# Performance work log

Hardware: AMD Instinct MI355X
Metric: run time of the kernel (lower is better)

The kernel has to match this reference:

```python
import jax, jax.numpy as jnp
import numpy as np

B, D, NSTEPS = 256, 4096, 30
DT = 0.5  # args.dt

def rho(x):
    # hard-sigmoid activation used throughout the EP repo
    return jnp.clip(x, 0.0, 1.0)

def setup_inputs() -> dict:
    key = jax.random.key(0)
    k_s3, k_w0, k_w2, k_w4 = jax.random.split(key, 4)
    sc = 1.0 / np.sqrt(D)
    W0 = jax.random.normal(k_w0, (D, D), jnp.float32) * sc  # w[0]: layer1 -> layer0
    W2 = jax.random.normal(k_w2, (D, D), jnp.float32) * sc  # w[2]: layer2 -> layer1
    W4 = jax.random.normal(k_w4, (D, D), jnp.float32) * sc  # w[4]: data  -> layer2
    return {
        "s0": jnp.zeros((B, D), jnp.float32),
        "s1": jnp.zeros((B, D), jnp.float32),
        "s2": jnp.zeros((B, D), jnp.float32),
        "s3": jax.random.uniform(k_s3, (B, D), jnp.float32),  # clamped data layer in [0,1]
        "W0": W0, "b0": jnp.zeros((D,), jnp.float32),
        "W1": W0.T,  # w[2i+1].weight = w[2i].weight.T at init (tied transpose)
        "W2": W2, "b2": jnp.zeros((D,), jnp.float32),
        "W3": W2.T,
        "W4": W4, "b4": jnp.zeros((D,), jnp.float32),
        "N": NSTEPS,
    }

def reference(s0, s1, s2, s3, W0, b0, W1, W2, b2, W3, W4, b4, N):
    # non-spiking EP free-phase relaxation (beta=0), no_clamp=False
    top_in = rho(s3) @ W4.T + b4  # s3 is clamped data; constant across steps

    def step(carry, _):
        c0, c1, c2 = carry
        r0, r1, r2 = rho(c0), rho(c1), rho(c2)
        ds0 = -c0 + r1 @ W0.T + b0
        ds1 = -c1 + r2 @ W2.T + b2 + r0 @ W1.T
        ds2 = -c2 + top_in + r1 @ W3.T
        n0 = jnp.clip(c0 + DT * ds0, 0.0, 1.0)
        n1 = jnp.clip(c1 + DT * ds1, 0.0, 1.0)
        n2 = jnp.clip(c2 + DT * ds2, 0.0, 1.0)
        return (n0, n1, n2), None

    (s0, s1, s2), _ = jax.lax.scan(step, (s0, s1, s2), None, length=N)
    return jnp.stack([s0, s1, s2])  # [3, B, D]
```

## Files before the change

### kernel.cpp

```cpp
#include <hip/hip_runtime.h>


typedef unsigned short u16;
typedef __attribute__((ext_vector_type(8))) _Float16 f16x8;
typedef __attribute__((ext_vector_type(4))) float f32x4;

constexpr int Bb = 256, Dd = 4096, NSTEPS = 30;
constexpr long BD = (long)Bb * Dd;
constexpr long DD = (long)Dd * Dd;
constexpr int BM = 32;
constexpr int NBUF = 3;
constexpr int BUFB = 20480;

__device__ inline u16 f2h(float f) { union { _Float16 h; u16 u; } v; v.h = (_Float16)f; return v.u; }
__device__ inline float h2f(u16 b) { union { u16 u; _Float16 h; } v; v.u = b; return (float)v.h; }

__device__ inline void gl_lds16(const u16* g, void* l) {
    __builtin_amdgcn_global_load_lds(
        (const __attribute__((address_space(1))) void*)g,
        (__attribute__((address_space(3))) void*)l, 16, 0, 0);
}

__global__ __launch_bounds__(256)
void convert_w(const float* __restrict__ src, u16* __restrict__ dst, long n) {
    long i = (long)blockIdx.x * blockDim.x + threadIdx.x;
    const long stride = (long)gridDim.x * blockDim.x;
    for (long v = i; v < (n >> 2); v += stride) {
        float4 x = ((const float4*)src)[v];
        ushort4 o; o.x = f2h(x.x); o.y = f2h(x.y); o.z = f2h(x.z); o.w = f2h(x.w);
        ((ushort4*)dst)[v] = o;
    }
}

__global__ __launch_bounds__(256)
void convert_s(const float* __restrict__ src, u16* __restrict__ hi, u16* __restrict__ lo, long n) {
    long i = (long)blockIdx.x * blockDim.x + threadIdx.x;
    const long stride = (long)gridDim.x * blockDim.x;
    for (long v = i; v < (n >> 2); v += stride) {
        float4 x = ((const float4*)src)[v];
        float a[4] = {x.x, x.y, x.z, x.w};
        ushort4 oh, ol;
        u16* ph = (u16*)&oh; u16* pl = (u16*)&ol;
        #pragma unroll
        for (int j = 0; j < 4; ++j) {
            float c = fminf(fmaxf(a[j], 0.f), 1.f);
            u16 hb = f2h(c);
            ph[j] = hb;
            pl[j] = f2h(c - h2f(hb));
        }
        ((ushort4*)hi)[v] = oh;
        ((ushort4*)lo)[v] = ol;
    }
}

__device__ inline void stage_tile(const u16* aH, const u16* aL, const u16* W,
                                  int m0, int n0, int k, char* buf, int wv, int lane)
{
    const int srow = lane >> 2;
    const int koff = (((lane & 3) ^ ((lane >> 3) & 3)) << 3);
    const u16* aBase = (wv < 2) ? aH : aL;
    const int aRow = ((wv & 1) << 4) + srow;
    char* aDst = buf + ((wv >> 1) << 11) + ((wv & 1) << 10);
    gl_lds16(aBase + (size_t)(m0 + aRow) * Dd + k + koff, aDst);
    const u16* wSrc = W + (size_t)(n0 + 64 * wv + srow) * Dd + k + koff;
    char* wDst = buf + 4096 + wv * 4096;
    #pragma unroll
    for (int c = 0; c < 4; ++c)
        gl_lds16(wSrc + (size_t)(16 * c) * Dd, wDst + (c << 10));
}

template<bool FULL>
__device__ inline void run_gemm(const u16* aH, const u16* aL, const u16* W,
                                const int m0, const int n0, char* smem,
                                const float* bias, const float* add,
                                const float* pF, const u16* pH, const u16* pL,
                                float* outF, u16* oH, u16* oL, const long zOff)
{
    const int lane = threadIdx.x & 63, wv = threadIdx.x >> 6;
    f32x4 acc[2][4] = {};
    constexpr int nk = 128;

    stage_tile(aH, aL, W, m0, n0, 0,  smem,        wv, lane);
    stage_tile(aH, aL, W, m0, n0, 32, smem + BUFB, wv, lane);

    int ib = 0;
    const int r16 = lane & 15;
    const int qoff = (((lane >> 4) ^ ((r16 >> 1) & 3)) << 4);

    for (int kk = 0; kk < nk; ++kk) {
        if (kk + 1 < nk) asm volatile("s_waitcnt vmcnt(5)" ::: "memory");
        else             asm volatile("s_waitcnt vmcnt(0)" ::: "memory");
        __builtin_amdgcn_s_barrier();
        asm volatile("" ::: "memory");

        if (kk + 2 < nk) {
            int ib2 = ib + 2; if (ib2 >= NBUF) ib2 -= NBUF;
            stage_tile(aH, aL, W, m0, n0, (kk + 2) << 5, smem + ib2 * BUFB, wv, lane);
        }

        const char* buf = smem + ib * BUFB;
        ++ib; if (ib == NBUF) ib = 0;

        f16x8 ah[2], al[2], wf[4];
        #pragma unroll
        for (int i = 0; i < 2; ++i) {
            ah[i] = *(const f16x8*)(buf + ((16 * i + r16) << 6) + qoff);
            al[i] = *(const f16x8*)(buf + 2048 + ((16 * i + r16) << 6) + qoff);
        }
        #pragma unroll
        for (int j = 0; j < 4; ++j)
            wf[j] = *(const f16x8*)(buf + 4096 + ((64 * wv + 16 * j + r16) << 6) + qoff);

        __builtin_amdgcn_s_setprio(1);
        #pragma unroll
        for (int j = 0; j < 4; ++j) {
            #pragma unroll
            for (int i = 0; i < 2; ++i) {
                acc[i][j] = __builtin_amdgcn_mfma_f32_16x16x32_f16(ah[i], wf[j], acc[i][j], 0, 0, 0);
                acc[i][j] = __builtin_amdgcn_mfma_f32_16x16x32_f16(al[i], wf[j], acc[i][j], 0, 0, 0);
            }
        }
        __builtin_amdgcn_s_setprio(0);
    }

    const int q = lane >> 4;
    #pragma unroll
    for (int j = 0; j < 4; ++j) {
        const int n = n0 + 64 * wv + 16 * j + r16;
        #pragma unroll
        for (int i = 0; i < 2; ++i) {
            #pragma unroll
            for (int r = 0; r < 4; ++r) {
                const int m = m0 + 16 * i + q * 4 + r;
                const size_t idx = (size_t)m * Dd + n;
                float e = acc[i][j][r];
                if (!FULL) {
                    outF[idx] = bias ? e + bias[n] : e;
                } else {
                    if (bias) e += bias[n];
                    if (add)  e += add[idx];
                    const float p = pF ? pF[zOff + idx] : (h2f(pH[zOff + idx]) + h2f(pL[zOff + idx]));
                    float v = 0.5f * p + 0.5f * e;
                    v = fminf(fmaxf(v, 0.f), 1.f);
                    const u16 hb = f2h(v);
                    oH[zOff + idx] = hb;
                    oL[zOff + idx] = f2h(v - h2f(hb));
                    if (outF) outF[zOff + idx] = v;
                }
            }
        }
    }
}

template<int MODE>
__global__ __launch_bounds__(256, 2)
void step_mfma(const u16* __restrict__ sH, const u16* __restrict__ sL,
               const u16* __restrict__ W0h, const u16* __restrict__ W1h,
               const u16* __restrict__ W2h, const u16* __restrict__ W3h,
               const float* __restrict__ b0, const float* __restrict__ b2,
               const float* __restrict__ top,
               const float* __restrict__ pF,
               const u16* __restrict__ pH, const u16* __restrict__ pL,
               float* __restrict__ outF,
               u16* __restrict__ oH, u16* __restrict__ oL,
               float* __restrict__ p0, float* __restrict__ p1)
{
    __shared__ __align__(16) char smem[NBUF * BUFB];
    const int id = blockIdx.x;

    if (MODE == 0) {
        const int mt = id >> 4, nt = id & 15;
        run_gemm<false>(sH, sL, W0h, mt * BM, nt * 256, smem, b0, nullptr,
                        nullptr, nullptr, nullptr, outF, nullptr, nullptr, 0);
    } else {
        const int t = id & 127, mt = t >> 4, nt = t & 15;
        const int m0 = mt * BM, n0 = nt * 256;
        if (id < 128) {
            run_gemm<true>(sH + BD, sL + BD, W0h, m0, n0, smem, b0, nullptr,
                           pF, pH, pL, outF, oH, oL, 0);
        } else if (id < 256) {
            run_gemm<false>(sH + 2 * BD, sL + 2 * BD, W2h, m0, n0, smem, b2, nullptr,
                            nullptr, nullptr, nullptr, p0, nullptr, nullptr, 0);
        } else if (id < 384) {
            run_gemm<false>(sH, sL, W1h, m0, n0, smem, nullptr, nullptr,
                            nullptr, nullptr, nullptr, p1, nullptr, nullptr, 0);
        } else {
            run_gemm<true>(sH + BD, sL + BD, W3h, m0, n0, smem, nullptr, top,
                           pF, pH, pL, outF, oH, oL, 2 * BD);
        }
    }
}

__global__ __launch_bounds__(256)
void finish_l1(const float* __restrict__ p0, const float* __restrict__ p1,
               const float* __restrict__ pF,
               const u16* __restrict__ pH, const u16* __restrict__ pL,
               float* __restrict__ outF, u16* __restrict__ oH, u16* __restrict__ oL)
{
    const long v = (long)blockIdx.x * blockDim.x + threadIdx.x;
    float4 a = ((const float4*)p0)[v];
    float4 b = ((const float4*)p1)[v];
    float e[4] = {a.x + b.x, a.y + b.y, a.z + b.z, a.w + b.w};
    float p[4];
    if (pF) {
        float4 pv = ((const float4*)(pF + BD))[v];
        p[0] = pv.x; p[1] = pv.y; p[2] = pv.z; p[3] = pv.w;
    } else {
        ushort4 hv = ((const ushort4*)(pH + BD))[v];
        ushort4 lv = ((const ushort4*)(pL + BD))[v];
        p[0] = h2f(hv.x) + h2f(lv.x); p[1] = h2f(hv.y) + h2f(lv.y);
        p[2] = h2f(hv.z) + h2f(lv.z); p[3] = h2f(hv.w) + h2f(lv.w);
    }
    ushort4 oh, ol; u16* ph = (u16*)&oh; u16* pl = (u16*)&ol;
    float4 ov;
    float* po = (float*)&ov;
    #pragma unroll
    for (int j = 0; j < 4; ++j) {
        float x = 0.5f * p[j] + 0.5f * e[j];
        x = fminf(fmaxf(x, 0.f), 1.f);
        const u16 hb = f2h(x);
        ph[j] = hb;
        pl[j] = f2h(x - h2f(hb));
        po[j] = x;
    }
    ((ushort4*)(oH + BD))[v] = oh;
    ((ushort4*)(oL + BD))[v] = ol;
    if (outF) ((float4*)(outF + BD))[v] = ov;
}

extern "C" void kernel_launch(void* const* d_in, const int* in_sizes, int n_in,
                              void* d_out, int out_size, void* d_ws, size_t ws_size,
                              hipStream_t stream)
{
    const float* s0 = (const float*)d_in[0];
    const float* s1 = (const float*)d_in[1];
    const float* s2 = (const float*)d_in[2];
    const float* s3 = (const float*)d_in[3];
    const float* W0 = (const float*)d_in[4];
    const float* b0 = (const float*)d_in[5];
    const float* W1 = (const float*)d_in[6];
    const float* W2 = (const float*)d_in[7];
    const float* b2 = (const float*)d_in[8];
    const float* W3 = (const float*)d_in[9];
    const float* W4 = (const float*)d_in[10];
    const float* b4 = (const float*)d_in[11];

    float* top = (float*)d_ws;
    u16* u   = (u16*)(top + BD);
    u16* W0h = u;            u16* W1h = u + DD;     u16* W2h = u + 2 * DD;
    u16* W3h = u + 3 * DD;   u16* W4h = u + 4 * DD;
    u16* sHa = u + 5 * DD;
    u16* sLa = sHa + 3 * BD;
    u16* sHb = sLa + 3 * BD;
    u16* sLb = sHb + 3 * BD;
    u16* s3h = sLb + 3 * BD;
    u16* s3l = s3h + BD;
    float* p0 = (float*)W4h;
    float* p1 = p0 + BD;

    float* out = (float*)d_out;
    const dim3 blk(256);
    const dim3 cgrid(512);

    convert_w<<<cgrid, blk, 0, stream>>>(W0, W0h, DD);
    convert_w<<<cgrid, blk, 0, stream>>>(W1, W1h, DD);
    convert_w<<<cgrid, blk, 0, stream>>>(W2, W2h, DD);
    convert_w<<<cgrid, blk, 0, stream>>>(W3, W3h, DD);
    convert_w<<<cgrid, blk, 0, stream>>>(W4, W4h, DD);
    convert_s<<<cgrid, blk, 0, stream>>>(s3, s3h, s3l, BD);
    convert_s<<<cgrid, blk, 0, stream>>>(s0, sHa,          sLa,          BD);
    convert_s<<<cgrid, blk, 0, stream>>>(s1, sHa + BD,     sLa + BD,     BD);
    convert_s<<<cgrid, blk, 0, stream>>>(s2, sHa + 2 * BD, sLa + 2 * BD, BD);

    step_mfma<0><<<dim3(128), blk, 0, stream>>>(
        s3h, s3l, W4h, nullptr, nullptr, nullptr,
        b4, nullptr, nullptr,
        nullptr, nullptr, nullptr,
        top, nullptr, nullptr, nullptr, nullptr);

    for (int t = 0; t < NSTEPS; ++t) {
        const u16* iH = (t & 1) ? sHb : sHa;
        const u16* iL = (t & 1) ? sLb : sLa;
        u16*       vH = (t & 1) ? sHa : sHb;
        u16*       vL = (t & 1) ? sLa : sLb;
        float* oF = (t == NSTEPS - 1) ? out : nullptr;
        const float* pF = nullptr;
        if (t == 0) {
            hipMemcpyAsync(out,          s0, BD * sizeof(float), hipMemcpyDeviceToDevice, stream);
            hipMemcpyAsync(out + BD,     s1, BD * sizeof(float), hipMemcpyDeviceToDevice, stream);
            hipMemcpyAsync(out + 2 * BD, s2, BD * sizeof(float), hipMemcpyDeviceToDevice, stream);
            pF = out;
        }
        step_mfma<1><<<dim3(512), blk, 0, stream>>>(
            iH, iL, W0h, W1h, W2h, W3h, b0, b2, top,
            pF, iH, iL,
            oF, vH, vL, p0, p1);
        finish_l1<<<dim3(BD / 4 / 256), blk, 0, stream>>>(
            p0, p1, pF, iH, iL, oF, vH, vL);
    }
}
```

Baseline: 3.758 ms.

## Load weight fragments directly to registers, stage only activations through LDS

Each wave's private W columns are now loaded straight from global memory into registers, double-buffered across iterations. Only the hi/lo activation tiles pass through LDS, with a new XOR swizzle. The K step grows from 32 to 64, halving the number of iterations and barriers, and the LDS buffer shrinks. The aim is to cut LDS traffic and space for W, since no wave shares it. The cost is more VGPR pressure from the register-held W fragments, and W global loads that are less coalesced and whose latency is exposed.

```diff
diff --git a/kernel.cpp b/kernel.cpp
--- a/kernel.cpp
+++ b/kernel.cpp
@@ -10,7 +10,7 @@
 constexpr long DD = (long)Dd * Dd;
 constexpr int BM = 32;
 constexpr int NBUF = 3;
-constexpr int BUFB = 20480;
+constexpr int BUFB = 8192;
 
 __device__ inline u16 f2h(float f) { union { _Float16 h; u16 u; } v; v.h = (_Float16)f; return v.u; }
 __device__ inline float h2f(u16 b) { union { u16 u; _Float16 h; } v; v.u = b; return (float)v.h; }
@@ -53,22 +53,6 @@
     }
 }
 
-__device__ inline void stage_tile(const u16* aH, const u16* aL, const u16* W,
-                                  int m0, int n0, int k, char* buf, int wv, int lane)
-{
-    const int srow = lane >> 2;
-    const int koff = (((lane & 3) ^ ((lane >> 3) & 3)) << 3);
-    const u16* aBase = (wv < 2) ? aH : aL;
-    const int aRow = ((wv & 1) << 4) + srow;
-    char* aDst = buf + ((wv >> 1) << 11) + ((wv & 1) << 10);
-    gl_lds16(aBase + (size_t)(m0 + aRow) * Dd + k + koff, aDst);
-    const u16* wSrc = W + (size_t)(n0 + 64 * wv + srow) * Dd + k + koff;
-    char* wDst = buf + 4096 + wv * 4096;
-    #pragma unroll
-    for (int c = 0; c < 4; ++c)
-        gl_lds16(wSrc + (size_t)(16 * c) * Dd, wDst + (c << 10));
-}
-
 template<bool FULL>
 __device__ inline void run_gemm(const u16* aH, const u16* aL, const u16* W,
                                 const int m0, const int n0, char* smem,
@@ -77,53 +61,90 @@
                                 float* outF, u16* oH, u16* oL, const long zOff)
 {
     const int lane = threadIdx.x & 63, wv = threadIdx.x >> 6;
+    const int r16 = lane & 15, q = lane >> 4;
     f32x4 acc[2][4] = {};
-    constexpr int nk = 128;
-
-    stage_tile(aH, aL, W, m0, n0, 0,  smem,        wv, lane);
-    stage_tile(aH, aL, W, m0, n0, 32, smem + BUFB, wv, lane);
+    constexpr int nk = 64;
+
+    const u16* wp[4];
+    #pragma unroll
+    for (int j = 0; j < 4; ++j)
+        wp[j] = W + (size_t)(n0 + 64 * wv + 16 * j + r16) * Dd + q * 8;
+
+    const int arow = 8 * wv + (lane >> 3);
+    const int aswz = ((lane & 7) ^ (lane >> 3)) * 8;
+    const u16* aSrcH = aH + (size_t)(m0 + arow) * Dd + aswz;
+    const u16* aSrcL = aL + (size_t)(m0 + arow) * Dd + aswz;
+
+    int aoff[2][2];
+    #pragma unroll
+    for (int i = 0; i < 2; ++i)
+        #pragma unroll
+        for (int h = 0; h < 2; ++h)
+            aoff[i][h] = (16 * i + r16) * 128 + (((4 * h + q) ^ (r16 & 7)) << 4);
 
     int ib = 0;
-    const int r16 = lane & 15;
-    const int qoff = (((lane >> 4) ^ ((r16 >> 1) & 3)) << 4);
-
-    for (int kk = 0; kk < nk; ++kk) {
-        if (kk + 1 < nk) asm volatile("s_waitcnt vmcnt(5)" ::: "memory");
-        else             asm volatile("s_waitcnt vmcnt(0)" ::: "memory");
+    f16x8 wfA[4][2], wfB[4][2];
+
+    auto stageA = [&](int kt, char* buf) {
+        gl_lds16(aSrcH + 64 * kt, buf + (wv << 10));
+        gl_lds16(aSrcL + 64 * kt, buf + 4096 + (wv << 10));
+    };
+
+    auto body = [&](int kk, f16x8 (&wfC)[4][2], f16x8 (&wfN)[4][2]) {
+        if (kk <= nk - 2) asm volatile("s_waitcnt vmcnt(10)" ::: "memory");
+        else              asm volatile("s_waitcnt vmcnt(8)"  ::: "memory");
         __builtin_amdgcn_s_barrier();
         asm volatile("" ::: "memory");
 
+        if (kk + 1 < nk) {
+            const int ko = 64 * (kk + 1);
+            #pragma unroll
+            for (int j = 0; j < 4; ++j)
+                #pragma unroll
+                for (int h = 0; h < 2; ++h)
+                    wfN[j][h] = *(const f16x8*)(wp[j] + ko + 32 * h);
+        }
         if (kk + 2 < nk) {
             int ib2 = ib + 2; if (ib2 >= NBUF) ib2 -= NBUF;
-            stage_tile(aH, aL, W, m0, n0, (kk + 2) << 5, smem + ib2 * BUFB, wv, lane);
+            stageA(kk + 2, smem + ib2 * BUFB);
         }
 
         const char* buf = smem + ib * BUFB;
         ++ib; if (ib == NBUF) ib = 0;
 
-        f16x8 ah[2], al[2], wf[4];
-        #pragma unroll
-        for (int i = 0; i < 2; ++i) {
-            ah[i] = *(const f16x8*)(buf + ((16 * i + r16) << 6) + qoff);
-            al[i] = *(const f16x8*)(buf + 2048 + ((16 * i + r16) << 6) + qoff);
-        }
-        #pragma unroll
-        for (int j = 0; j < 4; ++j)
-            wf[j] = *(const f16x8*)(buf + 4096 + ((64 * wv + 16 * j + r16) << 6) + qoff);
-
         __builtin_amdgcn_s_setprio(1);
         #pragma unroll
-        for (int j = 0; j < 4; ++j) {
+        for (int h = 0; h < 2; ++h) {
+            f16x8 ah[2], al[2];
             #pragma unroll
             for (int i = 0; i < 2; ++i) {
-                acc[i][j] = __builtin_amdgcn_mfma_f32_16x16x32_f16(ah[i], wf[j], acc[i][j], 0, 0, 0);
-                acc[i][j] = __builtin_amdgcn_mfma_f32_16x16x32_f16(al[i], wf[j], acc[i][j], 0, 0, 0);
+                ah[i] = *(const f16x8*)(buf + aoff[i][h]);
+                al[i] = *(const f16x8*)(buf + 4096 + aoff[i][h]);
             }
+            #pragma unroll
+            for (int j = 0; j < 4; ++j)
+                #pragma unroll
+                for (int i = 0; i < 2; ++i) {
+                    acc[i][j] = __builtin_amdgcn_mfma_f32_16x16x32_f16(ah[i], wfC[j][h], acc[i][j], 0, 0, 0);
+                    acc[i][j] = __builtin_amdgcn_mfma_f32_16x16x32_f16(al[i], wfC[j][h], acc[i][j], 0, 0, 0);
+                }
         }
         __builtin_amdgcn_s_setprio(0);
-    }
-
-    const int q = lane >> 4;
+    };
+
+    stageA(0, smem);
+    stageA(1, smem + BUFB);
+    #pragma unroll
+    for (int j = 0; j < 4; ++j)
+        #pragma unroll
+        for (int h = 0; h < 2; ++h)
+            wfA[j][h] = *(const f16x8*)(wp[j] + 32 * h);
+
+    for (int kk2 = 0; kk2 < nk; kk2 += 2) {
+        body(kk2,     wfA, wfB);
+        body(kk2 + 1, wfB, wfA);
+    }
+
     #pragma unroll
     for (int j = 0; j < 4; ++j) {
         const int n = n0 + 64 * wv + 16 * j + r16;
```

Result: slower. 4.934 ms (+31.3%).
